# Kernel tuning notes

Measured on AMD Instinct MI355X. Metric: run time of the kernel, lower is better.

Reference implementation:

```python
import jax, jax.numpy as jnp
import numpy as np

N = 100000
E = 1600000
IN_C = 128
HEADS = 4
HEAD_D = 32  # out_channels(128) // heads(4)


def setup_inputs() -> dict:
    key = jax.random.key(0)
    k1, k2, k3, k4, k5, k6 = jax.random.split(key, 6)
    x = jax.random.normal(k1, (N, IN_C), dtype=jnp.float32)
    edge_index = jax.random.randint(k2, (2, E), 0, N, dtype=jnp.int64)
    edge_weight = jax.random.uniform(k3, (E,), dtype=jnp.float32)
    # params: linear weight stored as [in, H*D] so forward is x @ W (torch does x @ weight.T)
    W = jax.random.normal(k4, (IN_C, HEADS * HEAD_D), dtype=jnp.float32) * (1.0 / np.sqrt(IN_C))
    att_src = jax.random.normal(k5, (HEADS, HEAD_D), dtype=jnp.float32) * 0.1
    att_dst = jax.random.normal(k6, (HEADS, HEAD_D), dtype=jnp.float32) * 0.1
    return {"x": x, "W": W, "att_src": att_src, "att_dst": att_dst,
            "edge_weight": edge_weight, "edge_index": edge_index, "num_nodes": N}


def reference(x, W, att_src, att_dst, edge_weight, edge_index, num_nodes):
    H, D = att_src.shape
    xw = (x @ W).reshape(-1, H, D)                       # [N, H, D]
    row, col = edge_index[0], edge_index[1]
    a_src = jnp.einsum('nhd,hd->nh', xw, att_src)        # [N, H]
    a_dst = jnp.einsum('nhd,hd->nh', xw, att_dst)        # [N, H]
    alpha = jax.nn.leaky_relu(a_src[row] + a_dst[col], negative_slope=0.2)  # [E, H]
    # segment softmax over edges grouped by row (destination of aggregation)
    amax = jax.ops.segment_max(alpha, row, num_segments=num_nodes)          # [N, H]
    amax = jnp.where(jnp.isfinite(amax), amax, 0.0)      # empty segments -> 0 (matches torch init)
    alpha = jnp.exp(alpha - amax[row])
    asum = jax.ops.segment_sum(alpha, row, num_segments=num_nodes)          # [N, H]
    alpha = alpha / (asum[row] + 1e-16)
    msg = xw[col] * alpha[..., None]                     # [E, H, D]
    out = jax.ops.segment_sum(msg, row, num_segments=num_nodes)             # [N, H, D]
    return out.reshape(num_nodes, H * D)
```

## Files before the change

### kernel.cpp

```cpp
#include <hip/hip_runtime.h>
#include <math.h>


typedef _Float16 half4 __attribute__((ext_vector_type(4)));
typedef _Float16 half8 __attribute__((ext_vector_type(8)));
typedef float    f32x4 __attribute__((ext_vector_type(4)));

#define PCHUNK   4096
#define NB_SHIFT 8
#define BCAP     4864

__device__ __forceinline__ float lrelu_exp(float v) {
    return __expf(fmaxf(v, 0.2f * v));
}

__global__ __launch_bounds__(128) void k_prep(const float* __restrict__ W,
                                              _Float16* __restrict__ WTh) {
    int n = blockIdx.x;
    int k = threadIdx.x;
    WTh[n * 128 + k] = (_Float16)W[(size_t)k * 128 + n];
}

__device__ __forceinline__ _Float16* lds_ptr(_Float16* base, int r, int kf16) {
    int g = (kf16 >> 3) ^ (r & 7);
    return base + r * 128 + g * 8 + (kf16 & 7);
}

__global__ __launch_bounds__(256) void k_gemm(const float* __restrict__ x,
                                              const _Float16* __restrict__ WTh,
                                              const float* __restrict__ att_src,
                                              const float* __restrict__ att_dst,
                                              _Float16* __restrict__ xwh,
                                              float* __restrict__ a_src,
                                              float* __restrict__ a_dst, int N) {
    __shared__ _Float16 Xs[128 * 128];
    __shared__ _Float16 Ws[128 * 128];
    int t = threadIdx.x;
    int lane = t & 63, wv = t >> 6;
    int lm = lane & 15, lg = lane >> 4;
    int row0 = blockIdx.x * 128;

    #pragma unroll
    for (int i = 0; i < 8; ++i) {
        int f = (i * 256 + t) * 8;
        int nr = f >> 7, kc = f & 127;
        *(half8*)lds_ptr(Ws, nr, kc) = *(const half8*)&WTh[f];
    }
    #pragma unroll
    for (int i = 0; i < 8; ++i) {
        int f = (i * 256 + t) * 8;
        int r = f >> 7, kc = f & 127;
        int gr = row0 + r; if (gr >= N) gr = N - 1;
        float4 v0 = *(const float4*)&x[(size_t)gr * 128 + kc];
        float4 v1 = *(const float4*)&x[(size_t)gr * 128 + kc + 4];
        half8 hv;
        hv[0] = (_Float16)v0.x; hv[1] = (_Float16)v0.y;
        hv[2] = (_Float16)v0.z; hv[3] = (_Float16)v0.w;
        hv[4] = (_Float16)v1.x; hv[5] = (_Float16)v1.y;
        hv[6] = (_Float16)v1.z; hv[7] = (_Float16)v1.w;
        *(half8*)lds_ptr(Xs, r, kc) = hv;
    }
    __syncthreads();

    f32x4 acc[2][8];
    #pragma unroll
    for (int m = 0; m < 2; ++m)
        #pragma unroll
        for (int nn = 0; nn < 8; ++nn) acc[m][nn] = (f32x4){0.f, 0.f, 0.f, 0.f};

    #pragma unroll
    for (int kk = 0; kk < 4; ++kk) {
        int kb = kk * 32 + lg * 8;
        half8 a0 = *(const half8*)lds_ptr(Xs, wv * 32 + lm, kb);
        half8 a1 = *(const half8*)lds_ptr(Xs, wv * 32 + 16 + lm, kb);
        half8 b[8];
        #pragma unroll
        for (int nn = 0; nn < 8; ++nn)
            b[nn] = *(const half8*)lds_ptr(Ws, nn * 16 + lm, kb);
        #pragma unroll
        for (int nn = 0; nn < 8; ++nn) {
            acc[0][nn] = __builtin_amdgcn_mfma_f32_16x16x32_f16(a0, b[nn], acc[0][nn], 0, 0, 0);
            acc[1][nn] = __builtin_amdgcn_mfma_f32_16x16x32_f16(a1, b[nn], acc[1][nn], 0, 0, 0);
        }
    }

    float asv[8], adv[8];
    #pragma unroll
    for (int nn = 0; nn < 8; ++nn) {
        asv[nn] = att_src[nn * 16 + lm];
        adv[nn] = att_dst[nn * 16 + lm];
    }
    #pragma unroll
    for (int m = 0; m < 2; ++m) {
        #pragma unroll
        for (int reg = 0; reg < 4; ++reg) {
            int row = row0 + wv * 32 + m * 16 + lg * 4 + reg;
            bool ok = row < N;
            if (ok) {
                #pragma unroll
                for (int nn = 0; nn < 8; ++nn)
                    xwh[(size_t)row * 128 + nn * 16 + lm] = (_Float16)acc[m][nn][reg];
            }
            float ps[4], pd[4];
            #pragma unroll
            for (int hh = 0; hh < 4; ++hh) {
                ps[hh] = acc[m][2 * hh][reg] * asv[2 * hh] + acc[m][2 * hh + 1][reg] * asv[2 * hh + 1];
                pd[hh] = acc[m][2 * hh][reg] * adv[2 * hh] + acc[m][2 * hh + 1][reg] * adv[2 * hh + 1];
                #pragma unroll
                for (int off = 1; off < 16; off <<= 1) {
                    ps[hh] += __shfl_xor(ps[hh], off);
                    pd[hh] += __shfl_xor(pd[hh], off);
                }
            }
            if (ok && lm == 0) {
                f32x4 vs = {ps[0], ps[1], ps[2], ps[3]};
                f32x4 vd = {pd[0], pd[1], pd[2], pd[3]};
                *(f32x4*)&a_src[(size_t)row * 4] = vs;
                *(f32x4*)&a_dst[(size_t)row * 4] = vd;
            }
        }
    }
}

__global__ __launch_bounds__(256) void k_part(const int* __restrict__ eidx,
                                              int* __restrict__ bctr,
                                              unsigned long long* __restrict__ rec,
                                              int E) {
    __shared__ unsigned long long buf[PCHUNK];
    __shared__ unsigned long long sbuf[PCHUNK];
    __shared__ int hist[512], excl[512], gbase[512], cur[512];
    __shared__ int wtot[4];
    int t = threadIdx.x;
    int lane = t & 63, wv = t >> 6;
    int e0 = blockIdx.x * PCHUNK;
    int nE = E - e0; if (nE > PCHUNK) nE = PCHUNK;
    hist[t] = 0; hist[t + 256] = 0;
    __syncthreads();
    for (int i = t; i < nE; i += 256) {
        int row = __builtin_nontemporal_load(&eidx[e0 + i]);
        int col = __builtin_nontemporal_load(&eidx[E + e0 + i]);
        buf[i] = ((unsigned long long)(unsigned)col << 32) | (unsigned)row;
        atomicAdd(&hist[row >> NB_SHIFT], 1);
    }
    __syncthreads();
    int h0 = hist[2 * t], h1 = hist[2 * t + 1];
    int s = h0 + h1, sc = s;
    #pragma unroll
    for (int off = 1; off < 64; off <<= 1) {
        int v = __shfl_up(sc, off);
        if (lane >= off) sc += v;
    }
    if (lane == 63) wtot[wv] = sc;
    __syncthreads();
    if (t == 0) {
        int run = 0;
        #pragma unroll
        for (int i = 0; i < 4; ++i) { int tmp = wtot[i]; wtot[i] = run; run += tmp; }
    }
    __syncthreads();
    int incl = sc + wtot[wv];
    excl[2 * t]     = incl - s;
    excl[2 * t + 1] = incl - h1;
    cur[2 * t]      = incl - s;
    cur[2 * t + 1]  = incl - h1;
    gbase[2 * t]     = h0 ? atomicAdd(&bctr[2 * t], h0) : 0;
    gbase[2 * t + 1] = h1 ? atomicAdd(&bctr[2 * t + 1], h1) : 0;
    __syncthreads();
    for (int i = t; i < nE; i += 256) {
        unsigned long long r = buf[i];
        int row = (int)(unsigned)r;
        int dst = atomicAdd(&cur[row >> NB_SHIFT], 1);
        sbuf[dst] = r;
    }
    __syncthreads();
    for (int j = t; j < nE; j += 256) {
        unsigned long long r = sbuf[j];
        int row = (int)(unsigned)r;
        int b = row >> NB_SHIFT;
        int off = gbase[b] + (j - excl[b]);
        if (off < BCAP)
            __builtin_nontemporal_store(r, &rec[(size_t)b * BCAP + off]);
    }
}

__global__ __launch_bounds__(256) void k_csr(const unsigned long long* __restrict__ rec,
                                             const int* __restrict__ bctr,
                                             int2* __restrict__ rseg,
                                             int* __restrict__ csr_col, int N) {
    __shared__ int cnt[256], cur[256];
    __shared__ int wtot[4];
    int b = blockIdx.x;
    int rs = b << NB_SHIFT;
    int t = threadIdx.x;
    int lane = t & 63, wv = t >> 6;
    cnt[t] = 0;
    __syncthreads();
    int m = bctr[b]; if (m > BCAP) m = BCAP;
    const unsigned long long* rr = &rec[(size_t)b * BCAP];
    for (int i = t; i < m; i += 256) {
        int row = (int)(unsigned)rr[i];
        atomicAdd(&cnt[row & 255], 1);
    }
    __syncthreads();
    int c = cnt[t], sc = c;
    #pragma unroll
    for (int off = 1; off < 64; off <<= 1) {
        int v = __shfl_up(sc, off);
        if (lane >= off) sc += v;
    }
    if (lane == 63) wtot[wv] = sc;
    __syncthreads();
    if (t == 0) {
        int run = 0;
        #pragma unroll
        for (int i = 0; i < 4; ++i) { int tmp = wtot[i]; wtot[i] = run; run += tmp; }
    }
    __syncthreads();
    int ex = sc + wtot[wv] - c;
    cur[t] = ex;
    int n = rs + t;
    if (n < N) {
        int2 sg;
        sg.x = b * BCAP + ex;
        sg.y = b * BCAP + ex + c;
        rseg[n] = sg;
    }
    __syncthreads();
    for (int i = t; i < m; i += 256) {
        unsigned long long r = rr[i];
        int row = (int)(unsigned)r;
        int col = (int)(r >> 32);
        int slot = atomicAdd(&cur[row & 255], 1);
        csr_col[b * BCAP + slot] = col;
    }
}

#define EDGE4(C0, C1, C2, C3, M0, M1, M2, M3)                              \
    {                                                                      \
        float ad0 = a_dst[(size_t)(C0) * 4 + h];                           \
        float ad1 = a_dst[(size_t)(C1) * 4 + h];                           \
        float ad2 = a_dst[(size_t)(C2) * 4 + h];                           \
        float ad3 = a_dst[(size_t)(C3) * 4 + h];                           \
        half8 x0 = *(const half8*)&xwh[(size_t)(C0) * 128 + (l << 3)];     \
        half8 x1 = *(const half8*)&xwh[(size_t)(C1) * 128 + (l << 3)];     \
        half8 x2 = *(const half8*)&xwh[(size_t)(C2) * 128 + (l << 3)];     \
        half8 x3 = *(const half8*)&xwh[(size_t)(C3) * 128 + (l << 3)];     \
        float w0 = (M0) * lrelu_exp(s + ad0);                              \
        float w1 = (M1) * lrelu_exp(s + ad1);                              \
        float w2 = (M2) * lrelu_exp(s + ad2);                              \
        float w3 = (M3) * lrelu_exp(s + ad3);                              \
        ws += w0 + w1 + w2 + w3;                                           \
        _Pragma("unroll")                                                  \
        for (int kk = 0; kk < 8; ++kk)                                     \
            acc[kk] += w0 * (float)x0[kk] + w1 * (float)x1[kk]             \
                     + w2 * (float)x2[kk] + w3 * (float)x3[kk];            \
    }

#define FETCH2(IDX) ({ int _i = (IDX);                                     \
                       int _c0 = __shfl(cc0, _i);                          \
                       int _c1 = __shfl(cc1, _i - 64);                     \
                       _i < 64 ? _c0 : _c1; })

__global__ __launch_bounds__(256) void k_agg(const int2* __restrict__ rseg,
                                             const int* __restrict__ csr_col,
                                             const float* __restrict__ a_src,
                                             const float* __restrict__ a_dst,
                                             const _Float16* __restrict__ xwh,
                                             float* __restrict__ out, int N) {
    int lane = threadIdx.x & 63;
    int wv = threadIdx.x >> 6;
    int n0 = (blockIdx.x * 4 + wv) * 4;
    if (n0 >= N) return;
    int nv = N - n0; if (nv > 4) nv = 4;
    int q = lane >> 4;
    int l = lane & 15;
    int h = l >> 2;

    int begs[4], ends[4];
    if (nv == 4) {
        int4 sa = *(const int4*)&rseg[n0];
        int4 sb = *(const int4*)&rseg[n0 + 2];
        begs[0] = sa.x; ends[0] = sa.y; begs[1] = sa.z; ends[1] = sa.w;
        begs[2] = sb.x; ends[2] = sb.y; begs[3] = sb.z; ends[3] = sb.w;
    } else {
        int2 s0 = rseg[n0];
        begs[0] = s0.x; ends[0] = s0.y;
        #pragma unroll
        for (int j = 1; j < 4; ++j) {
            if (j < nv) { int2 sj = rseg[n0 + j]; begs[j] = sj.x; ends[j] = sj.y; }
            else        { begs[j] = ends[j - 1];  ends[j] = ends[j - 1]; }
        }
    }
    float sn[4];
    #pragma unroll
    for (int j = 0; j < 4; ++j)
        sn[j] = (j < nv) ? a_src[(size_t)(n0 + j) * 4 + h] : 0.f;

    int base = begs[0];
    int L = ends[3] - base;

    if (L <= 128) {
        int cc0 = (lane < L)      ? __builtin_nontemporal_load(&csr_col[base + lane])      : 0;
        int cc1 = (lane + 64 < L) ? __builtin_nontemporal_load(&csr_col[base + 64 + lane]) : 0;
        #pragma unroll
        for (int j = 0; j < 4; ++j) {
            float acc[8] = {0, 0, 0, 0, 0, 0, 0, 0};
            float ws = 0.f;
            float s = sn[j];
            int deg = ends[j] - begs[j];
            int o = begs[j] - base;
            int i = 0;
            for (; i + 16 <= deg; i += 16) {
                int i0 = o + i + q;
                int c0 = FETCH2(i0);
                int c1 = FETCH2(i0 + 4);
                int c2 = FETCH2(i0 + 8);
                int c3 = FETCH2(i0 + 12);
                EDGE4(c0, c1, c2, c3, 1.f, 1.f, 1.f, 1.f);
            }
            if (i < deg) {
                int r0 = i + q, r1 = i + 4 + q, r2 = i + 8 + q, r3 = i + 12 + q;
                float m0 = r0 < deg ? 1.f : 0.f;
                float m1 = r1 < deg ? 1.f : 0.f;
                float m2 = r2 < deg ? 1.f : 0.f;
                float m3 = r3 < deg ? 1.f : 0.f;
                int c0 = FETCH2(r0 < deg ? o + r0 : o);
                int c1 = FETCH2(r1 < deg ? o + r1 : o);
                int c2 = FETCH2(r2 < deg ? o + r2 : o);
                int c3 = FETCH2(r3 < deg ? o + r3 : o);
                EDGE4(c0, c1, c2, c3, m0, m1, m2, m3);
            }
            #pragma unroll
            for (int kk = 0; kk < 8; ++kk) {
                acc[kk] += __shfl_xor(acc[kk], 16);
                acc[kk] += __shfl_xor(acc[kk], 32);
            }
            ws += __shfl_xor(ws, 16);
            ws += __shfl_xor(ws, 32);
            if (q == 0 && j < nv) {
                int n = n0 + j;
                float inv = 1.0f / (ws + 1e-16f);
                f32x4 o0 = {acc[0] * inv, acc[1] * inv, acc[2] * inv, acc[3] * inv};
                f32x4 o1 = {acc[4] * inv, acc[5] * inv, acc[6] * inv, acc[7] * inv};
                __builtin_nontemporal_store(o0, (f32x4*)&out[(size_t)n * 128 + (l << 3)]);
                __builtin_nontemporal_store(o1, (f32x4*)&out[(size_t)n * 128 + (l << 3) + 4]);
            }
        }
    } else {
        #pragma unroll
        for (int j = 0; j < 4; ++j) {
            float acc[8] = {0, 0, 0, 0, 0, 0, 0, 0};
            float ws = 0.f;
            float s = sn[j];
            int beg = begs[j], end = ends[j];
            for (int w0 = beg; w0 < end; w0 += 64) {
                int rem = end - w0; if (rem > 64) rem = 64;
                int cc = (lane < rem) ? __builtin_nontemporal_load(&csr_col[w0 + lane]) : 0;
                int i = 0;
                for (; i + 16 <= rem; i += 16) {
                    int c0 = __shfl(cc, i + q);
                    int c1 = __shfl(cc, i + 4 + q);
                    int c2 = __shfl(cc, i + 8 + q);
                    int c3 = __shfl(cc, i + 12 + q);
                    EDGE4(c0, c1, c2, c3, 1.f, 1.f, 1.f, 1.f);
                }
                if (i < rem) {
                    int r0 = i + q, r1 = i + 4 + q, r2 = i + 8 + q, r3 = i + 12 + q;
                    float m0 = r0 < rem ? 1.f : 0.f;
                    float m1 = r1 < rem ? 1.f : 0.f;
                    float m2 = r2 < rem ? 1.f : 0.f;
                    float m3 = r3 < rem ? 1.f : 0.f;
                    int c0 = __shfl(cc, r0);
                    int c1 = __shfl(cc, r1);
                    int c2 = __shfl(cc, r2);
                    int c3 = __shfl(cc, r3);
                    EDGE4(c0, c1, c2, c3, m0, m1, m2, m3);
                }
            }
            #pragma unroll
            for (int kk = 0; kk < 8; ++kk) {
                acc[kk] += __shfl_xor(acc[kk], 16);
                acc[kk] += __shfl_xor(acc[kk], 32);
            }
            ws += __shfl_xor(ws, 16);
            ws += __shfl_xor(ws, 32);
            if (q == 0 && j < nv) {
                int n = n0 + j;
                float inv = 1.0f / (ws + 1e-16f);
                f32x4 o0 = {acc[0] * inv, acc[1] * inv, acc[2] * inv, acc[3] * inv};
                f32x4 o1 = {acc[4] * inv, acc[5] * inv, acc[6] * inv, acc[7] * inv};
                __builtin_nontemporal_store(o0, (f32x4*)&out[(size_t)n * 128 + (l << 3)]);
                __builtin_nontemporal_store(o1, (f32x4*)&out[(size_t)n * 128 + (l << 3) + 4]);
            }
        }
    }
}

extern "C" void kernel_launch(void* const* d_in, const int* in_sizes, int n_in,
                              void* d_out, int out_size, void* d_ws, size_t ws_size,
                              hipStream_t stream) {
    const float* x       = (const float*)d_in[0];
    const float* W       = (const float*)d_in[1];
    const float* att_src = (const float*)d_in[2];
    const float* att_dst = (const float*)d_in[3];
    const int* eidx      = (const int*)d_in[5];
    int N = in_sizes[0] / 128;
    int E = in_sizes[4];
    float* out = (float*)d_out;

    char* p = (char*)d_ws;
    auto alloc = [&](size_t bytes) {
        char* r = p;
        p += (bytes + 255) & ~(size_t)255;
        return r;
    };
    int nbuckets = (N + 255) >> NB_SHIFT;
    _Float16* xwh  = (_Float16*)alloc((size_t)N * 128 * 2);
    float* a_src   = (float*)alloc((size_t)N * 4 * 4);
    float* a_dst   = (float*)alloc((size_t)N * 4 * 4);
    int*   bctr    = (int*)  alloc(512 * 4);
    unsigned long long* rec = (unsigned long long*)alloc((size_t)nbuckets * BCAP * 8);
    int2*  rseg    = (int2*) alloc((size_t)N * 8);
    int*   csr_col = (int*)  alloc((size_t)nbuckets * BCAP * 4);
    _Float16* WTh  = (_Float16*)alloc(128 * 128 * 2);

    (void)hipMemsetAsync(bctr, 0, 512 * 4, stream);
    k_prep<<<128, 128, 0, stream>>>(W, WTh);
    k_gemm<<<(N + 127) / 128, 256, 0, stream>>>(x, WTh, att_src, att_dst, xwh, a_src, a_dst, N);
    k_part<<<(E + PCHUNK - 1) / PCHUNK, 256, 0, stream>>>(eidx, bctr, rec, E);
    k_csr<<<nbuckets, 256, 0, stream>>>(rec, bctr, rseg, csr_col, N);
    k_agg<<<(N + 15) / 16, 256, 0, stream>>>(rseg, csr_col, a_src, a_dst, xwh, out, N);
}
```

Measured before the change: 247.7 us.

## Stage gathered neighbor features into LDS via async global_load_lds in aggregation

Rewrites the aggregation kernel so each 256-thread block handles 16 rows with a shared edge list. Neighbor feature rows are staged into LDS with direct global-to-LDS async loads, and per-edge attention weights are computed once per edge and head. Each thread then accumulates one row's 8 channels from LDS, with no cross-lane shuffle reductions. This adds block-wide barriers, a 32KB+ LDS footprint that limits occupancy, and serialized per-thread accumulation over a row's edges.

```diff
diff --git a/kernel.cpp b/kernel.cpp
--- a/kernel.cpp
+++ b/kernel.cpp
@@ -9,6 +9,9 @@
 #define PCHUNK   4096
 #define NB_SHIFT 8
 #define BCAP     4864
+
+#define AGG_ROWS 16
+#define AGG_CAP  128
 
 __device__ __forceinline__ float lrelu_exp(float v) {
     return __expf(fmaxf(v, 0.2f * v));
@@ -235,164 +238,99 @@
     }
 }
 
-#define EDGE4(C0, C1, C2, C3, M0, M1, M2, M3)                              \
-    {                                                                      \
-        float ad0 = a_dst[(size_t)(C0) * 4 + h];                           \
-        float ad1 = a_dst[(size_t)(C1) * 4 + h];                           \
-        float ad2 = a_dst[(size_t)(C2) * 4 + h];                           \
-        float ad3 = a_dst[(size_t)(C3) * 4 + h];                           \
-        half8 x0 = *(const half8*)&xwh[(size_t)(C0) * 128 + (l << 3)];     \
-        half8 x1 = *(const half8*)&xwh[(size_t)(C1) * 128 + (l << 3)];     \
-        half8 x2 = *(const half8*)&xwh[(size_t)(C2) * 128 + (l << 3)];     \
-        half8 x3 = *(const half8*)&xwh[(size_t)(C3) * 128 + (l << 3)];     \
-        float w0 = (M0) * lrelu_exp(s + ad0);                              \
-        float w1 = (M1) * lrelu_exp(s + ad1);                              \
-        float w2 = (M2) * lrelu_exp(s + ad2);                              \
-        float w3 = (M3) * lrelu_exp(s + ad3);                              \
-        ws += w0 + w1 + w2 + w3;                                           \
-        _Pragma("unroll")                                                  \
-        for (int kk = 0; kk < 8; ++kk)                                     \
-            acc[kk] += w0 * (float)x0[kk] + w1 * (float)x1[kk]             \
-                     + w2 * (float)x2[kk] + w3 * (float)x3[kk];            \
-    }
-
-#define FETCH2(IDX) ({ int _i = (IDX);                                     \
-                       int _c0 = __shfl(cc0, _i);                          \
-                       int _c1 = __shfl(cc1, _i - 64);                     \
-                       _i < 64 ? _c0 : _c1; })
-
 __global__ __launch_bounds__(256) void k_agg(const int2* __restrict__ rseg,
                                              const int* __restrict__ csr_col,
                                              const float* __restrict__ a_src,
                                              const float* __restrict__ a_dst,
                                              const _Float16* __restrict__ xwh,
                                              float* __restrict__ out, int N) {
-    int lane = threadIdx.x & 63;
-    int wv = threadIdx.x >> 6;
-    int n0 = (blockIdx.x * 4 + wv) * 4;
-    if (n0 >= N) return;
-    int nv = N - n0; if (nv > 4) nv = 4;
-    int q = lane >> 4;
-    int l = lane & 15;
-    int h = l >> 2;
-
-    int begs[4], ends[4];
-    if (nv == 4) {
-        int4 sa = *(const int4*)&rseg[n0];
-        int4 sb = *(const int4*)&rseg[n0 + 2];
-        begs[0] = sa.x; ends[0] = sa.y; begs[1] = sa.z; ends[1] = sa.w;
-        begs[2] = sb.x; ends[2] = sb.y; begs[3] = sb.z; ends[3] = sb.w;
-    } else {
-        int2 s0 = rseg[n0];
-        begs[0] = s0.x; ends[0] = s0.y;
-        #pragma unroll
-        for (int j = 1; j < 4; ++j) {
-            if (j < nv) { int2 sj = rseg[n0 + j]; begs[j] = sj.x; ends[j] = sj.y; }
-            else        { begs[j] = ends[j - 1];  ends[j] = ends[j - 1]; }
-        }
-    }
-    float sn[4];
-    #pragma unroll
-    for (int j = 0; j < 4; ++j)
-        sn[j] = (j < nv) ? a_src[(size_t)(n0 + j) * 4 + h] : 0.f;
-
-    int base = begs[0];
-    int L = ends[3] - base;
-
-    if (L <= 128) {
-        int cc0 = (lane < L)      ? __builtin_nontemporal_load(&csr_col[base + lane])      : 0;
-        int cc1 = (lane + 64 < L) ? __builtin_nontemporal_load(&csr_col[base + 64 + lane]) : 0;
-        #pragma unroll
-        for (int j = 0; j < 4; ++j) {
-            float acc[8] = {0, 0, 0, 0, 0, 0, 0, 0};
-            float ws = 0.f;
-            float s = sn[j];
-            int deg = ends[j] - begs[j];
-            int o = begs[j] - base;
-            int i = 0;
-            for (; i + 16 <= deg; i += 16) {
-                int i0 = o + i + q;
-                int c0 = FETCH2(i0);
-                int c1 = FETCH2(i0 + 4);
-                int c2 = FETCH2(i0 + 8);
-                int c3 = FETCH2(i0 + 12);
-                EDGE4(c0, c1, c2, c3, 1.f, 1.f, 1.f, 1.f);
-            }
-            if (i < deg) {
-                int r0 = i + q, r1 = i + 4 + q, r2 = i + 8 + q, r3 = i + 12 + q;
-                float m0 = r0 < deg ? 1.f : 0.f;
-                float m1 = r1 < deg ? 1.f : 0.f;
-                float m2 = r2 < deg ? 1.f : 0.f;
-                float m3 = r3 < deg ? 1.f : 0.f;
-                int c0 = FETCH2(r0 < deg ? o + r0 : o);
-                int c1 = FETCH2(r1 < deg ? o + r1 : o);
-                int c2 = FETCH2(r2 < deg ? o + r2 : o);
-                int c3 = FETCH2(r3 < deg ? o + r3 : o);
-                EDGE4(c0, c1, c2, c3, m0, m1, m2, m3);
-            }
+    __shared__ _Float16 Xg[AGG_CAP * 128];
+    __shared__ float    wls[AGG_CAP][4];
+    __shared__ int      cols[AGG_CAP];
+    __shared__ int      bounds[AGG_ROWS + 1];
+    int t = threadIdx.x;
+    int lane = t & 63, wv = t >> 6;
+    int row0 = blockIdx.x * AGG_ROWS;
+
+    if (t <= AGG_ROWS) {
+        int lastr = N - 1;
+        int v;
+        if (t == AGG_ROWS) {
+            int er = row0 + AGG_ROWS - 1;
+            v = rseg[er <= lastr ? er : lastr].y;
+        } else {
+            int rr = row0 + t;
+            v = (rr <= lastr) ? rseg[rr].x : rseg[lastr].y;
+        }
+        bounds[t] = v;
+    }
+
+    int my_r = t >> 4;
+    int my_c = t & 15;
+    int my_h = my_c >> 2;
+    int gr = row0 + my_r;
+    float acc[8] = {0, 0, 0, 0, 0, 0, 0, 0};
+    float ws = 0.f;
+    __syncthreads();
+    int beg = bounds[0], end = bounds[AGG_ROWS];
+    int myb = bounds[my_r], mye = bounds[my_r + 1];
+
+    for (int cb = beg; cb < end; cb += AGG_CAP) {
+        int cnt = end - cb; if (cnt > AGG_CAP) cnt = AGG_CAP;
+        if (cb != beg) __syncthreads();
+        if (t < cnt) cols[t] = csr_col[cb + t];
+        __syncthreads();
+
+        int nI = (cnt + 3) >> 2;
+        for (int ii = wv; ii < nI; ii += 4) {
+            int e = ii * 4 + (lane >> 4);
+            int ec = e < cnt ? e : cnt - 1;
+            int c = cols[ec];
+            const _Float16* gp = xwh + (size_t)c * 128 + (lane & 15) * 8;
+            __builtin_amdgcn_global_load_lds(
+                (const __attribute__((address_space(1))) void*)gp,
+                (__attribute__((address_space(3))) void*)(Xg + ii * 512),
+                16, 0, 0);
+        }
+        for (int i = t; i < cnt; i += 256) {
+            int c = cols[i];
+            int eg = cb + i;
+            int r = 0;
+            if (bounds[r + 8] <= eg) r += 8;
+            if (bounds[r + 4] <= eg) r += 4;
+            if (bounds[r + 2] <= eg) r += 2;
+            if (bounds[r + 1] <= eg) r += 1;
+            float4 ad = *(const float4*)&a_dst[(size_t)c * 4];
+            float4 as = *(const float4*)&a_src[(size_t)(row0 + r) * 4];
+            f32x4 w4;
+            w4[0] = lrelu_exp(as.x + ad.x);
+            w4[1] = lrelu_exp(as.y + ad.y);
+            w4[2] = lrelu_exp(as.z + ad.z);
+            w4[3] = lrelu_exp(as.w + ad.w);
+            *(f32x4*)&wls[i][0] = w4;
+        }
+        asm volatile("s_waitcnt vmcnt(0)" ::: "memory");
+        __syncthreads();
+
+        int lo = (myb > cb ? myb : cb) - cb;
+        int hi = (mye < cb + cnt ? mye : cb + cnt) - cb;
+        #pragma unroll 2
+        for (int e = lo; e < hi; ++e) {
+            float w = wls[e][my_h];
+            half8 xv = *(const half8*)&Xg[e * 128 + my_c * 8];
+            ws += w;
             #pragma unroll
-            for (int kk = 0; kk < 8; ++kk) {
-                acc[kk] += __shfl_xor(acc[kk], 16);
-                acc[kk] += __shfl_xor(acc[kk], 32);
-            }
-            ws += __shfl_xor(ws, 16);
-            ws += __shfl_xor(ws, 32);
-            if (q == 0 && j < nv) {
-                int n = n0 + j;
-                float inv = 1.0f / (ws + 1e-16f);
-                f32x4 o0 = {acc[0] * inv, acc[1] * inv, acc[2] * inv, acc[3] * inv};
-                f32x4 o1 = {acc[4] * inv, acc[5] * inv, acc[6] * inv, acc[7] * inv};
-                __builtin_nontemporal_store(o0, (f32x4*)&out[(size_t)n * 128 + (l << 3)]);
-                __builtin_nontemporal_store(o1, (f32x4*)&out[(size_t)n * 128 + (l << 3) + 4]);
-            }
-        }
-    } else {
-        #pragma unroll
-        for (int j = 0; j < 4; ++j) {
-            float acc[8] = {0, 0, 0, 0, 0, 0, 0, 0};
-            float ws = 0.f;
-            float s = sn[j];
-            int beg = begs[j], end = ends[j];
-            for (int w0 = beg; w0 < end; w0 += 64) {
-                int rem = end - w0; if (rem > 64) rem = 64;
-                int cc = (lane < rem) ? __builtin_nontemporal_load(&csr_col[w0 + lane]) : 0;
-                int i = 0;
-                for (; i + 16 <= rem; i += 16) {
-                    int c0 = __shfl(cc, i + q);
-                    int c1 = __shfl(cc, i + 4 + q);
-                    int c2 = __shfl(cc, i + 8 + q);
-                    int c3 = __shfl(cc, i + 12 + q);
-                    EDGE4(c0, c1, c2, c3, 1.f, 1.f, 1.f, 1.f);
-                }
-                if (i < rem) {
-                    int r0 = i + q, r1 = i + 4 + q, r2 = i + 8 + q, r3 = i + 12 + q;
-                    float m0 = r0 < rem ? 1.f : 0.f;
-                    float m1 = r1 < rem ? 1.f : 0.f;
-                    float m2 = r2 < rem ? 1.f : 0.f;
-                    float m3 = r3 < rem ? 1.f : 0.f;
-                    int c0 = __shfl(cc, r0);
-                    int c1 = __shfl(cc, r1);
-                    int c2 = __shfl(cc, r2);
-                    int c3 = __shfl(cc, r3);
-                    EDGE4(c0, c1, c2, c3, m0, m1, m2, m3);
-                }
-            }
-            #pragma unroll
-            for (int kk = 0; kk < 8; ++kk) {
-                acc[kk] += __shfl_xor(acc[kk], 16);
-                acc[kk] += __shfl_xor(acc[kk], 32);
-            }
-            ws += __shfl_xor(ws, 16);
-            ws += __shfl_xor(ws, 32);
-            if (q == 0 && j < nv) {
-                int n = n0 + j;
-                float inv = 1.0f / (ws + 1e-16f);
-                f32x4 o0 = {acc[0] * inv, acc[1] * inv, acc[2] * inv, acc[3] * inv};
-                f32x4 o1 = {acc[4] * inv, acc[5] * inv, acc[6] * inv, acc[7] * inv};
-                __builtin_nontemporal_store(o0, (f32x4*)&out[(size_t)n * 128 + (l << 3)]);
-                __builtin_nontemporal_store(o1, (f32x4*)&out[(size_t)n * 128 + (l << 3) + 4]);
-            }
-        }
+            for (int j = 0; j < 8; ++j)
+                acc[j] += w * (float)xv[j];
+        }
+    }
+
+    if (gr < N) {
+        float inv = 1.0f / (ws + 1e-16f);
+        f32x4 o0 = {acc[0] * inv, acc[1] * inv, acc[2] * inv, acc[3] * inv};
+        f32x4 o1 = {acc[4] * inv, acc[5] * inv, acc[6] * inv, acc[7] * inv};
+        __builtin_nontemporal_store(o0, (f32x4*)&out[(size_t)gr * 128 + (my_c << 3)]);
+        __builtin_nontemporal_store(o1, (f32x4*)&out[(size_t)gr * 128 + (my_c << 3) + 4]);
     }
 }
 
@@ -429,5 +367,5 @@
     k_gemm<<<(N + 127) / 128, 256, 0, stream>>>(x, WTh, att_src, att_dst, xwh, a_src, a_dst, N);
     k_part<<<(E + PCHUNK - 1) / PCHUNK, 256, 0, stream>>>(eidx, bctr, rec, E);
     k_csr<<<nbuckets, 256, 0, stream>>>(rec, bctr, rseg, csr_col, N);
-    k_agg<<<(N + 15) / 16, 256, 0, stream>>>(rseg, csr_col, a_src, a_dst, xwh, out, N);
-}
+    k_agg<<<(N + AGG_ROWS - 1) / AGG_ROWS, 256, 0, stream>>>(rseg, csr_col, a_src, a_dst, xwh, out, N);
+}
```

New measurement: 250.1 us. About the same (+1.0%).
